# Optimization experiments

Measured on AMD Instinct MI355X. Metric: run time of the kernel, lower is better.

Reference implementation:

```python
import jax, jax.numpy as jnp
import numpy as np

NUM_COND = 16  # num_conditions
EPS = 1e-5


def setup_inputs() -> dict:
    key = jax.random.key(0)
    k1, k2, k3, k4 = jax.random.split(key, 4)
    N, F = 500000, 128
    x = jax.random.normal(k1, (N, F), dtype=jnp.float32)
    labels = jax.random.randint(k2, (N,), 0, NUM_COND)
    gamma = jax.random.uniform(k3, (NUM_COND, F), dtype=jnp.float32)
    beta = jax.random.normal(k4, (NUM_COND, F), dtype=jnp.float32)
    return {"x": x, "labels": labels, "gamma": gamma, "beta": beta}


def reference(x, labels, gamma, beta):
    # Conditional BatchNorm1d (training mode): per-label batch statistics
    # over the samples of each group, then per-label affine transform.
    num_cond = gamma.shape[0]
    ones = jnp.ones((x.shape[0],), x.dtype)
    counts = jax.ops.segment_sum(ones, labels, num_segments=num_cond)   # [C]
    counts = jnp.maximum(counts, 1.0)                                    # guard empty groups
    s1 = jax.ops.segment_sum(x, labels, num_segments=num_cond)          # [C,F]
    s2 = jax.ops.segment_sum(x * x, labels, num_segments=num_cond)      # [C,F]
    mean = s1 / counts[:, None]
    var = s2 / counts[:, None] - mean * mean                             # biased var (BatchNorm)
    inv_std = jax.lax.rsqrt(var + EPS)                                   # [C,F]
    scale = gamma * inv_std                                              # [C,F]
    shift = beta - mean * scale                                          # [C,F]
    y = x * scale[labels] + shift[labels]                                # fused gather + affine
    return y
```

## Files before the change

### kernel.cpp

```cpp
#include <hip/hip_runtime.h>

#define NUM_COND 16
#define FDIM 128
#define EPS 1e-5f
#define WPB 4
#define NSLOT 6
#define PB 4160
#define NCHUNK 16
#define MAXNB 512

typedef float __attribute__((ext_vector_type(4))) f4v;
__device__ __forceinline__ void nt_store4(float4* p, const float4& v) {
    f4v t = { v.x, v.y, v.z, v.w };
    __builtin_nontemporal_store(t, (f4v*)p);
}

__global__ __launch_bounds__(256) void cbn_stats_kernel(
    const float* __restrict__ x, const int* __restrict__ labels,
    float* __restrict__ ws, int N, int chunk)
{
    __shared__ float acc[WPB][4096];
    const int t = threadIdx.x;
    const int w = t >> 6;
    const int lane = t & 63;

    {
        float4* z = (float4*)acc[w];
        for (int i = lane; i < 1024; i += 64) z[i] = make_float4(0.f, 0.f, 0.f, 0.f);
    }

    const int rbeg = blockIdx.x * chunk;
    const int rend = min(N, rbeg + chunk);
    const float2* x2 = (const float2*)x;
    float2* r1 = (float2*)acc[w];
    float2* r2 = ((float2*)acc[w]) + 1024;

    int cnt = 0;
    float2 v0, v1, v2, v3, v4, v5;
    int lb0 = 0, lb1 = 0, lb2 = 0, lb3 = 0, lb4 = 0, lb5 = 0;
    v0 = v1 = v2 = v3 = v4 = v5 = make_float2(0.f, 0.f);

#define LOADSLOT(S, R)                                              \
    {   const int r_ = (R);                                         \
        if (r_ < rend) {                                            \
            v##S = x2[(size_t)r_ * 64 + lane];                      \
            lb##S = labels[r_];                                     \
        }                                                           \
    }

#define PROCSLOT(S, R)                                              \
    {   const int r_ = (R);                                         \
        if (r_ < rend) {                                            \
            const int o_ = lb##S * 64 + lane;                       \
            float2 o1 = r1[o_];                                     \
            float2 o2 = r2[o_];                                     \
            o1.x += v##S.x;                  o1.y += v##S.y;        \
            o2.x = fmaf(v##S.x, v##S.x, o2.x);                      \
            o2.y = fmaf(v##S.y, v##S.y, o2.y);                      \
            r1[o_] = o1;                                            \
            r2[o_] = o2;                                            \
            cnt += ((lane & 15) == lb##S) ? 1 : 0;                  \
        }                                                           \
    }

    int r = rbeg + w;
    LOADSLOT(0, r)
    LOADSLOT(1, r + WPB)
    LOADSLOT(2, r + 2 * WPB)
    LOADSLOT(3, r + 3 * WPB)
    LOADSLOT(4, r + 4 * WPB)
    LOADSLOT(5, r + 5 * WPB)

    for (; r < rend; r += NSLOT * WPB) {
        PROCSLOT(0, r)
        LOADSLOT(0, r + 6 * WPB)
        PROCSLOT(1, r + WPB)
        LOADSLOT(1, r + 7 * WPB)
        PROCSLOT(2, r + 2 * WPB)
        LOADSLOT(2, r + 8 * WPB)
        PROCSLOT(3, r + 3 * WPB)
        LOADSLOT(3, r + 9 * WPB)
        PROCSLOT(4, r + 4 * WPB)
        LOADSLOT(4, r + 10 * WPB)
        PROCSLOT(5, r + 5 * WPB)
        LOADSLOT(5, r + 11 * WPB)
    }

    __syncthreads();
    float* out = ws + (size_t)blockIdx.x * PB;
    for (int i = t; i < 4096; i += 256)
        out[i] = acc[0][i] + acc[1][i] + acc[2][i] + acc[3][i];
    if (lane < 16) out[4096 + w * 16 + lane] = (float)cnt;
}

__global__ __launch_bounds__(256) void cbn_reduce_kernel(
    const float* __restrict__ ws, float* __restrict__ ws2, int nb, int per)
{
    const int e = blockIdx.x * 256 + threadIdx.x;
    if (e >= PB) return;
    const int b0 = blockIdx.y * per;
    const int b1 = min(nb, b0 + per);
    float a = 0.f;
#pragma unroll 8
    for (int b = b0; b < b1; ++b) a += ws[(size_t)b * PB + e];
    ws2[(size_t)blockIdx.y * PB + e] = a;
}

__global__ __launch_bounds__(256) void cbn_finalize_kernel(
    const float* __restrict__ ws2, const float* __restrict__ gamma,
    const float* __restrict__ beta, float* __restrict__ scale_shift)
{
    const int e = blockIdx.x * 256 + threadIdx.x;
    const int lab = e >> 7;
    float a1 = 0.f, a2 = 0.f, cn = 0.f;
#pragma unroll
    for (int k = 0; k < NCHUNK; ++k) {
        const float* p = ws2 + (size_t)k * PB;
        a1 += p[e];
        a2 += p[2048 + e];
#pragma unroll
        for (int w2 = 0; w2 < WPB; ++w2)
            cn += p[4096 + w2 * 16 + lab];
    }
    cn = fmaxf(cn, 1.0f);
    const float mean = a1 / cn;
    const float var  = a2 / cn - mean * mean;
    const float sc = gamma[e] * rsqrtf(var + EPS);
    const float sh = beta[e] - mean * sc;
    scale_shift[e]        = sc;
    scale_shift[2048 + e] = sh;
}

__global__ __launch_bounds__(256) void cbn_apply_kernel(
    const float* __restrict__ x, const int* __restrict__ labels,
    const float* __restrict__ scale_shift, float* __restrict__ y, int N)
{
    __shared__ float4 ssc[NUM_COND * 32];
    __shared__ float4 ssh[NUM_COND * 32];
    const int t = threadIdx.x;
    const float4* ss4 = (const float4*)scale_shift;
    for (int i = t; i < NUM_COND * 32; i += 256) {
        ssc[i] = ss4[i];
        ssh[i] = ss4[512 + i];
    }
    __syncthreads();

    const int f4 = t & 31;
    const int rg = t >> 5;
    const float4* x4 = (const float4*)x;
    float4* y4 = (float4*)y;

    for (int base = blockIdx.x * 32 + rg; base < N; base += gridDim.x * 32) {
        const int r0 = base;
        int r1 = base + 8, r2 = base + 16, r3 = base + 24;
        const bool k1 = r1 < N, k2 = r2 < N, k3 = r3 < N;
        if (!k1) r1 = r0;  if (!k2) r2 = r0;  if (!k3) r3 = r0;

        const int l0 = labels[r0], l1 = labels[r1], l2 = labels[r2], l3 = labels[r3];
        const float4 v0 = x4[(size_t)r0 * 32 + f4];
        const float4 v1 = x4[(size_t)r1 * 32 + f4];
        const float4 v2 = x4[(size_t)r2 * 32 + f4];
        const float4 v3 = x4[(size_t)r3 * 32 + f4];

        const float4 c0 = ssc[l0 * 32 + f4], h0 = ssh[l0 * 32 + f4];
        const float4 c1 = ssc[l1 * 32 + f4], h1 = ssh[l1 * 32 + f4];
        const float4 c2 = ssc[l2 * 32 + f4], h2 = ssh[l2 * 32 + f4];
        const float4 c3 = ssc[l3 * 32 + f4], h3 = ssh[l3 * 32 + f4];

        float4 o0, o1, o2, o3;
        o0.x = fmaf(v0.x, c0.x, h0.x); o0.y = fmaf(v0.y, c0.y, h0.y);
        o0.z = fmaf(v0.z, c0.z, h0.z); o0.w = fmaf(v0.w, c0.w, h0.w);
        o1.x = fmaf(v1.x, c1.x, h1.x); o1.y = fmaf(v1.y, c1.y, h1.y);
        o1.z = fmaf(v1.z, c1.z, h1.z); o1.w = fmaf(v1.w, c1.w, h1.w);
        o2.x = fmaf(v2.x, c2.x, h2.x); o2.y = fmaf(v2.y, c2.y, h2.y);
        o2.z = fmaf(v2.z, c2.z, h2.z); o2.w = fmaf(v2.w, c2.w, h2.w);
        o3.x = fmaf(v3.x, c3.x, h3.x); o3.y = fmaf(v3.y, c3.y, h3.y);
        o3.z = fmaf(v3.z, c3.z, h3.z); o3.w = fmaf(v3.w, c3.w, h3.w);

        nt_store4(&y4[(size_t)r0 * 32 + f4], o0);
        if (k1) nt_store4(&y4[(size_t)r1 * 32 + f4], o1);
        if (k2) nt_store4(&y4[(size_t)r2 * 32 + f4], o2);
        if (k3) nt_store4(&y4[(size_t)r3 * 32 + f4], o3);
    }
}

extern "C" void kernel_launch(void* const* d_in, const int* in_sizes, int n_in,
                              void* d_out, int out_size, void* d_ws, size_t ws_size,
                              hipStream_t stream)
{
    const float* x      = (const float*)d_in[0];
    const int*   labels = (const int*)d_in[1];
    const float* gamma  = (const float*)d_in[2];
    const float* beta   = (const float*)d_in[3];
    float* y  = (float*)d_out;
    float* ws = (float*)d_ws;
    const int N = in_sizes[1];

    const long floats = (long)(ws_size / sizeof(float));
    long avail = floats - (long)NCHUNK * PB - 4096;
    int nb = MAXNB;
    if ((long)nb * PB > avail) nb = (int)(avail / PB);
    if (nb < 1) nb = 1;
    const int chunk = (N + nb - 1) / nb;
    const int per   = (nb + NCHUNK - 1) / NCHUNK;

    float* ws2         = ws + (size_t)nb * PB;
    float* scale_shift = ws2 + (size_t)NCHUNK * PB;

    cbn_stats_kernel<<<nb, 256, 0, stream>>>(x, labels, ws, N, chunk);
    cbn_reduce_kernel<<<dim3((PB + 255) / 256, NCHUNK), 256, 0, stream>>>(ws, ws2, nb, per);
    cbn_finalize_kernel<<<8, 256, 0, stream>>>(ws2, gamma, beta, scale_shift);
    cbn_apply_kernel<<<2048, 256, 0, stream>>>(x, labels, scale_shift, y, N);
}
```

Measured before the change: 137.6 us.

## Split stats accumulation into wave pairs computing sum and sum-of-squares separately

The stats kernel now runs 512 threads as four wave pairs. In each pair one wave accumulates the per-label sum and the other the sum of squares, each in its own 8 KB LDS region, so each wave does half the LDS read-modify-write work per row. The aim is more waves in flight to hide latency and less LDS work per wave. In exchange every row of x is loaded twice (once per wave in the pair), which raises L2 and global load traffic, and the block needs twice the threads.

After: 138.9 us. Within noise of the previous version (+1.0%).

```diff
diff --git a/kernel.cpp b/kernel.cpp
--- a/kernel.cpp
+++ b/kernel.cpp
@@ -3,7 +3,7 @@
 #define NUM_COND 16
 #define FDIM 128
 #define EPS 1e-5f
-#define WPB 4
+#define PAIRS 4
 #define NSLOT 6
 #define PB 4160
 #define NCHUNK 16
@@ -15,25 +15,26 @@
     __builtin_nontemporal_store(t, (f4v*)p);
 }
 
-__global__ __launch_bounds__(256) void cbn_stats_kernel(
+__global__ __launch_bounds__(512) void cbn_stats_kernel(
     const float* __restrict__ x, const int* __restrict__ labels,
     float* __restrict__ ws, int N, int chunk)
 {
-    __shared__ float acc[WPB][4096];
+    __shared__ float acc[2 * PAIRS][2048];
     const int t = threadIdx.x;
     const int w = t >> 6;
+    const int pair = w >> 1;
+    const int role = w & 1;
     const int lane = t & 63;
 
     {
         float4* z = (float4*)acc[w];
-        for (int i = lane; i < 1024; i += 64) z[i] = make_float4(0.f, 0.f, 0.f, 0.f);
+        for (int i = lane; i < 512; i += 64) z[i] = make_float4(0.f, 0.f, 0.f, 0.f);
     }
 
     const int rbeg = blockIdx.x * chunk;
     const int rend = min(N, rbeg + chunk);
     const float2* x2 = (const float2*)x;
-    float2* r1 = (float2*)acc[w];
-    float2* r2 = ((float2*)acc[w]) + 1024;
+    float2* rr = (float2*)acc[w];
 
     int cnt = 0;
     float2 v0, v1, v2, v3, v4, v5;
@@ -52,45 +53,46 @@
     {   const int r_ = (R);                                         \
         if (r_ < rend) {                                            \
             const int o_ = lb##S * 64 + lane;                       \
-            float2 o1 = r1[o_];                                     \
-            float2 o2 = r2[o_];                                     \
-            o1.x += v##S.x;                  o1.y += v##S.y;        \
-            o2.x = fmaf(v##S.x, v##S.x, o2.x);                      \
-            o2.y = fmaf(v##S.y, v##S.y, o2.y);                      \
-            r1[o_] = o1;                                            \
-            r2[o_] = o2;                                            \
+            const float mx = role ? v##S.x : 1.0f;                  \
+            const float my = role ? v##S.y : 1.0f;                  \
+            float2 o1 = rr[o_];                                     \
+            o1.x = fmaf(v##S.x, mx, o1.x);                          \
+            o1.y = fmaf(v##S.y, my, o1.y);                          \
+            rr[o_] = o1;                                            \
             cnt += ((lane & 15) == lb##S) ? 1 : 0;                  \
         }                                                           \
     }
 
-    int r = rbeg + w;
+    int r = rbeg + pair;
     LOADSLOT(0, r)
-    LOADSLOT(1, r + WPB)
-    LOADSLOT(2, r + 2 * WPB)
-    LOADSLOT(3, r + 3 * WPB)
-    LOADSLOT(4, r + 4 * WPB)
-    LOADSLOT(5, r + 5 * WPB)
-
-    for (; r < rend; r += NSLOT * WPB) {
+    LOADSLOT(1, r + PAIRS)
+    LOADSLOT(2, r + 2 * PAIRS)
+    LOADSLOT(3, r + 3 * PAIRS)
+    LOADSLOT(4, r + 4 * PAIRS)
+    LOADSLOT(5, r + 5 * PAIRS)
+
+    for (; r < rend; r += NSLOT * PAIRS) {
         PROCSLOT(0, r)
-        LOADSLOT(0, r + 6 * WPB)
-        PROCSLOT(1, r + WPB)
-        LOADSLOT(1, r + 7 * WPB)
-        PROCSLOT(2, r + 2 * WPB)
-        LOADSLOT(2, r + 8 * WPB)
-        PROCSLOT(3, r + 3 * WPB)
-        LOADSLOT(3, r + 9 * WPB)
-        PROCSLOT(4, r + 4 * WPB)
-        LOADSLOT(4, r + 10 * WPB)
-        PROCSLOT(5, r + 5 * WPB)
-        LOADSLOT(5, r + 11 * WPB)
+        LOADSLOT(0, r + 6 * PAIRS)
+        PROCSLOT(1, r + PAIRS)
+        LOADSLOT(1, r + 7 * PAIRS)
+        PROCSLOT(2, r + 2 * PAIRS)
+        LOADSLOT(2, r + 8 * PAIRS)
+        PROCSLOT(3, r + 3 * PAIRS)
+        LOADSLOT(3, r + 9 * PAIRS)
+        PROCSLOT(4, r + 4 * PAIRS)
+        LOADSLOT(4, r + 10 * PAIRS)
+        PROCSLOT(5, r + 5 * PAIRS)
+        LOADSLOT(5, r + 11 * PAIRS)
     }
 
     __syncthreads();
     float* out = ws + (size_t)blockIdx.x * PB;
-    for (int i = t; i < 4096; i += 256)
-        out[i] = acc[0][i] + acc[1][i] + acc[2][i] + acc[3][i];
-    if (lane < 16) out[4096 + w * 16 + lane] = (float)cnt;
+    for (int i = t; i < 2048; i += 512) {
+        out[i]        = acc[0][i] + acc[2][i] + acc[4][i] + acc[6][i];
+        out[2048 + i] = acc[1][i] + acc[3][i] + acc[5][i] + acc[7][i];
+    }
+    if (role == 0 && lane < 16) out[4096 + pair * 16 + lane] = (float)cnt;
 }
 
 __global__ __launch_bounds__(256) void cbn_reduce_kernel(
@@ -119,7 +121,7 @@
         a1 += p[e];
         a2 += p[2048 + e];
 #pragma unroll
-        for (int w2 = 0; w2 < WPB; ++w2)
+        for (int w2 = 0; w2 < PAIRS; ++w2)
             cn += p[4096 + w2 * 16 + lab];
     }
     cn = fmaxf(cn, 1.0f);
@@ -207,7 +209,7 @@
     float* ws2         = ws + (size_t)nb * PB;
     float* scale_shift = ws2 + (size_t)NCHUNK * PB;
 
-    cbn_stats_kernel<<<nb, 256, 0, stream>>>(x, labels, ws, N, chunk);
+    cbn_stats_kernel<<<nb, 512, 0, stream>>>(x, labels, ws, N, chunk);
     cbn_reduce_kernel<<<dim3((PB + 255) / 256, NCHUNK), 256, 0, stream>>>(ws, ws2, nb, per);
     cbn_finalize_kernel<<<8, 256, 0, stream>>>(ws2, gamma, beta, scale_shift);
     cbn_apply_kernel<<<2048, 256, 0, stream>>>(x, labels, scale_shift, y, N);
```

## Merge reduce and finalize kernels and deepen stats prefetch to eight slots

Applied to the files above, without the earlier changes.

Replaces the two-stage partial reduction (a reduce kernel into 16 chunks, then finalize) with a single 8-block kernel where each thread sums all nb per-block partials directly, with per-block counts summed once into shared memory. This removes one kernel launch and the intermediate workspace. The trade-off is that only 8 blocks now read 512 rows of partials serially, which exposes per-thread load latency. The stats kernel prefetch depth also goes from 6 to 8 rows per wave to keep more loads in flight, at some register cost.

After: 286.2 us. 108% more time.

```diff
diff --git a/kernel.cpp b/kernel.cpp
--- a/kernel.cpp
+++ b/kernel.cpp
@@ -4,9 +4,8 @@
 #define FDIM 128
 #define EPS 1e-5f
 #define WPB 4
-#define NSLOT 6
+#define NSLOT 8
 #define PB 4160
-#define NCHUNK 16
 #define MAXNB 512
 
 typedef float __attribute__((ext_vector_type(4))) f4v;
@@ -36,9 +35,9 @@
     float2* r2 = ((float2*)acc[w]) + 1024;
 
     int cnt = 0;
-    float2 v0, v1, v2, v3, v4, v5;
-    int lb0 = 0, lb1 = 0, lb2 = 0, lb3 = 0, lb4 = 0, lb5 = 0;
-    v0 = v1 = v2 = v3 = v4 = v5 = make_float2(0.f, 0.f);
+    float2 v0, v1, v2, v3, v4, v5, v6, v7;
+    int lb0 = 0, lb1 = 0, lb2 = 0, lb3 = 0, lb4 = 0, lb5 = 0, lb6 = 0, lb7 = 0;
+    v0 = v1 = v2 = v3 = v4 = v5 = v6 = v7 = make_float2(0.f, 0.f);
 
 #define LOADSLOT(S, R)                                              \
     {   const int r_ = (R);                                         \
@@ -70,20 +69,26 @@
     LOADSLOT(3, r + 3 * WPB)
     LOADSLOT(4, r + 4 * WPB)
     LOADSLOT(5, r + 5 * WPB)
+    LOADSLOT(6, r + 6 * WPB)
+    LOADSLOT(7, r + 7 * WPB)
 
     for (; r < rend; r += NSLOT * WPB) {
         PROCSLOT(0, r)
-        LOADSLOT(0, r + 6 * WPB)
+        LOADSLOT(0, r + 8 * WPB)
         PROCSLOT(1, r + WPB)
-        LOADSLOT(1, r + 7 * WPB)
+        LOADSLOT(1, r + 9 * WPB)
         PROCSLOT(2, r + 2 * WPB)
-        LOADSLOT(2, r + 8 * WPB)
+        LOADSLOT(2, r + 10 * WPB)
         PROCSLOT(3, r + 3 * WPB)
-        LOADSLOT(3, r + 9 * WPB)
+        LOADSLOT(3, r + 11 * WPB)
         PROCSLOT(4, r + 4 * WPB)
-        LOADSLOT(4, r + 10 * WPB)
+        LOADSLOT(4, r + 12 * WPB)
         PROCSLOT(5, r + 5 * WPB)
-        LOADSLOT(5, r + 11 * WPB)
+        LOADSLOT(5, r + 13 * WPB)
+        PROCSLOT(6, r + 6 * WPB)
+        LOADSLOT(6, r + 14 * WPB)
+        PROCSLOT(7, r + 7 * WPB)
+        LOADSLOT(7, r + 15 * WPB)
     }
 
     __syncthreads();
@@ -93,36 +98,35 @@
     if (lane < 16) out[4096 + w * 16 + lane] = (float)cnt;
 }
 
-__global__ __launch_bounds__(256) void cbn_reduce_kernel(
-    const float* __restrict__ ws, float* __restrict__ ws2, int nb, int per)
-{
-    const int e = blockIdx.x * 256 + threadIdx.x;
-    if (e >= PB) return;
-    const int b0 = blockIdx.y * per;
-    const int b1 = min(nb, b0 + per);
-    float a = 0.f;
+__global__ __launch_bounds__(256) void cbn_reduce_finalize_kernel(
+    const float* __restrict__ ws, const float* __restrict__ gamma,
+    const float* __restrict__ beta, float* __restrict__ scale_shift, int nb)
+{
+    __shared__ float scnt[WPB * 16];
+    const int t = threadIdx.x;
+    const int e = blockIdx.x * 256 + t;
+    const int lab = e >> 7;
+
+    if (t < WPB * 16) {
+        float c = 0.f;
 #pragma unroll 8
-    for (int b = b0; b < b1; ++b) a += ws[(size_t)b * PB + e];
-    ws2[(size_t)blockIdx.y * PB + e] = a;
-}
-
-__global__ __launch_bounds__(256) void cbn_finalize_kernel(
-    const float* __restrict__ ws2, const float* __restrict__ gamma,
-    const float* __restrict__ beta, float* __restrict__ scale_shift)
-{
-    const int e = blockIdx.x * 256 + threadIdx.x;
-    const int lab = e >> 7;
-    float a1 = 0.f, a2 = 0.f, cn = 0.f;
-#pragma unroll
-    for (int k = 0; k < NCHUNK; ++k) {
-        const float* p = ws2 + (size_t)k * PB;
+        for (int b = 0; b < nb; ++b) c += ws[(size_t)b * PB + 4096 + t];
+        scnt[t] = c;
+    }
+    __syncthreads();
+
+    float a1 = 0.f, a2 = 0.f;
+#pragma unroll 8
+    for (int b = 0; b < nb; ++b) {
+        const float* p = ws + (size_t)b * PB;
         a1 += p[e];
         a2 += p[2048 + e];
+    }
+    float cn = 0.f;
 #pragma unroll
-        for (int w2 = 0; w2 < WPB; ++w2)
-            cn += p[4096 + w2 * 16 + lab];
-    }
+    for (int w2 = 0; w2 < WPB; ++w2) cn += scnt[w2 * 16 + lab];
     cn = fmaxf(cn, 1.0f);
+
     const float mean = a1 / cn;
     const float var  = a2 / cn - mean * mean;
     const float sc = gamma[e] * rsqrtf(var + EPS);
@@ -197,18 +201,15 @@
     const int N = in_sizes[1];
 
     const long floats = (long)(ws_size / sizeof(float));
-    long avail = floats - (long)NCHUNK * PB - 4096;
+    long avail = floats - 4096;
     int nb = MAXNB;
     if ((long)nb * PB > avail) nb = (int)(avail / PB);
     if (nb < 1) nb = 1;
     const int chunk = (N + nb - 1) / nb;
-    const int per   = (nb + NCHUNK - 1) / NCHUNK;
-
-    float* ws2         = ws + (size_t)nb * PB;
-    float* scale_shift = ws2 + (size_t)NCHUNK * PB;
+
+    float* scale_shift = ws + (size_t)nb * PB;
 
     cbn_stats_kernel<<<nb, 256, 0, stream>>>(x, labels, ws, N, chunk);
-    cbn_reduce_kernel<<<dim3((PB + 255) / 256, NCHUNK), 256, 0, stream>>>(ws, ws2, nb, per);
-    cbn_finalize_kernel<<<8, 256, 0, stream>>>(ws2, gamma, beta, scale_shift);
+    cbn_reduce_finalize_kernel<<<8, 256, 0, stream>>>(ws, gamma, beta, scale_shift, nb);
     cbn_apply_kernel<<<2048, 256, 0, stream>>>(x, labels, scale_shift, y, N);
 }
```
